# Optimization experiments

Hardware: AMD Instinct MI355X
Metric: run time of the kernel (lower is better)

## Reference

```python
import jax, jax.numpy as jnp
import numpy as np

B, T, M, E = 2, 2048, 1024, 8
CAP = (2 * B * T) // E  # GShard top-2 capacity = 2*S/E = 1024


def setup_inputs() -> dict:
    key = jax.random.key(0)
    k1, k2, k3 = jax.random.split(key, 3)
    x = jax.random.normal(k1, (B, T, M), jnp.float32)
    wg = jax.random.normal(k2, (M, E), jnp.float32) * 0.02
    expert_w = jax.random.normal(k3, (E, M, M), jnp.float32) * 0.02
    expert_b = jnp.zeros((E, M), jnp.float32)
    return {"x": x, "wg": wg, "expert_w": expert_w, "expert_b": expert_b}


def _top2_gate(x2, wg, capacity):
    """fairseq/GShard Top2Gate (deterministic second-expert, no jitter).
    Returns (l_aux, combine_weights[S,E,C], dispatch_mask[S,E,C] bool)."""
    S = x2.shape[0]
    num_experts = wg.shape[1]
    logits = x2 @ wg                                  # [S, E]
    gates = jax.nn.softmax(logits, axis=-1)           # [S, E]
    # top-1 expert
    idx1 = jnp.argmax(gates, axis=1)
    mask1 = jax.nn.one_hot(idx1, num_experts, dtype=jnp.int32)
    # top-2 expert: argmax over logits with top-1 masked out
    neg_inf = jnp.finfo(logits.dtype).min
    logits_wo1 = jnp.where(mask1.astype(bool), neg_inf, logits)
    idx2 = jnp.argmax(logits_wo1, axis=1)
    mask2 = jax.nn.one_hot(idx2, num_experts, dtype=jnp.int32)
    # positions within each expert's buffer
    loc1 = jnp.cumsum(mask1, axis=0) - 1              # [S, E]
    loc2 = jnp.cumsum(mask2, axis=0) - 1 + jnp.sum(mask1, axis=0, keepdims=True)
    # load-balancing auxiliary loss
    me = jnp.mean(gates, axis=0)
    ce = jnp.mean(mask1.astype(gates.dtype), axis=0)
    l_aux = jnp.mean(me * ce) * (num_experts * num_experts)
    # drop tokens over capacity
    mask1 = mask1 * (loc1 < capacity).astype(jnp.int32)
    mask2 = mask2 * (loc2 < capacity).astype(jnp.int32)
    loc1_s = jnp.sum(loc1 * mask1, axis=1)            # [S]
    loc2_s = jnp.sum(loc2 * mask2, axis=1)
    m1f = mask1.astype(gates.dtype)
    m2f = mask2.astype(gates.dtype)
    gates1_s = jnp.sum(gates * m1f, axis=1)
    gates2_s = jnp.sum(gates * m2f, axis=1)
    denom = gates1_s + gates2_s
    denom = jnp.clip(denom, jnp.finfo(gates.dtype).eps, None)
    gates1 = gates1_s / denom
    gates2 = gates2_s / denom
    loc1_oh = jax.nn.one_hot(loc1_s, capacity, dtype=gates.dtype)  # [S, C]
    loc2_oh = jax.nn.one_hot(loc2_s, capacity, dtype=gates.dtype)
    combine1 = gates1[:, None, None] * m1f[:, :, None] * loc1_oh[:, None, :]
    combine2 = gates2[:, None, None] * m2f[:, :, None] * loc2_oh[:, None, :]
    combine_weights = combine1 + combine2             # [S, E, C]
    dispatch_mask = combine_weights > 0               # bool [S, E, C]
    return l_aux, combine_weights, dispatch_mask


def reference(x, wg, expert_w, expert_b):
    b, t, d = x.shape
    x2 = x.reshape(-1, d)                             # [S, M]
    l_aux, cw, dm = _top2_gate(x2, wg, CAP)
    dmf = dm.astype(x.dtype)                          # [S, E, C]
    # dispatch: (E*C, S) @ (S, M) -> per-expert token buffers [E, C, M]
    dispatched = jnp.einsum('sec,sm->ecm', dmf, x2)
    # per-expert Linear (single device: all experts local, all-to-all = identity)
    expert_out = jnp.einsum('ecm,emn->ecn', dispatched, expert_w) + expert_b[:, None, :]
    # combine: (S, E*C) @ (E*C, M) -> [S, M]
    combined = jnp.einsum('sec,ecm->sm', cw, expert_out)
    return combined.reshape(b, t, d), l_aux
```

## Files before the change

### kernel.cpp

```cpp
#include <hip/hip_runtime.h>

typedef unsigned short u16;
typedef short v8s __attribute__((ext_vector_type(8)));
typedef float v4f __attribute__((ext_vector_type(4)));

#define S_TOK 4096
#define MDIM  1024
#define NEXP  8
#define CAPN  1024

__device__ __forceinline__ u16 f2bf(float f) {
  unsigned int u = __float_as_uint(f);
  u += 0x7FFFu + ((u >> 16) & 1u);
  return (u16)(u >> 16);
}

__device__ __forceinline__ void gll16(const void* g, void* l) {
  __builtin_amdgcn_global_load_lds(
      (const __attribute__((address_space(1))) void*)g,
      (__attribute__((address_space(3))) void*)l, 16, 0, 0);
}

__global__ __launch_bounds__(256) void init_kernel(int* slot_token, u16* zrow, float* gsum) {
  int gid = blockIdx.x * 256 + threadIdx.x;
  if (gid < NEXP * CAPN) slot_token[gid] = -1;
  if (gid < MDIM) zrow[gid] = 0;
  if (gid < NEXP) gsum[gid] = 0.f;
}

__global__ __launch_bounds__(256) void transw_kernel(const float* __restrict__ w,
                                                     u16* __restrict__ wT) {
  int b  = blockIdx.x;
  int e  = b >> 8;
  int mt = (b >> 4) & 15;
  int nt = b & 15;
  __shared__ float tile[64][65];
  const float* src = w + (size_t)e * MDIM * MDIM;
  u16* dst = wT + (size_t)e * MDIM * MDIM;
  int tid = threadIdx.x;
#pragma unroll
  for (int i = 0; i < 16; i++) {
    int idx = tid + i * 256;
    int r = idx >> 6, c = idx & 63;
    tile[r][c] = src[(size_t)(mt * 64 + r) * MDIM + nt * 64 + c];
  }
  __syncthreads();
#pragma unroll
  for (int i = 0; i < 16; i++) {
    int idx = tid + i * 256;
    int r = idx >> 6, c = idx & 63;
    dst[(size_t)(nt * 64 + r) * MDIM + mt * 64 + c] = f2bf(tile[c][r]);
  }
}

__global__ __launch_bounds__(256) void gate_kernel(const float* __restrict__ x,
                                                   const float* __restrict__ wg,
                                                   u16* __restrict__ xbf,
                                                   int4* __restrict__ grec,
                                                   float* __restrict__ gsum) {
  __shared__ float wls[NEXP * MDIM];
  __shared__ float gsh[4][NEXP];
  int tid = threadIdx.x;
  for (int i = tid; i < NEXP * MDIM; i += 256) {
    int m = i >> 3, e = i & 7;
    wls[e * MDIM + m] = wg[i];
  }
  __syncthreads();
  int wave = tid >> 6, lane = tid & 63;
  int s = blockIdx.x * 4 + wave;
  const float* xr = x + (size_t)s * MDIM;
  u16* xw = xbf + (size_t)s * MDIM;
  float acc[NEXP];
#pragma unroll
  for (int e = 0; e < NEXP; e++) acc[e] = 0.f;
#pragma unroll
  for (int j = 0; j < 16; j++) {
    int m = j * 64 + lane;
    float xv = xr[m];
    xw[m] = f2bf(xv);
#pragma unroll
    for (int e = 0; e < NEXP; e++) acc[e] = fmaf(xv, wls[e * MDIM + m], acc[e]);
  }
#pragma unroll
  for (int off = 32; off > 0; off >>= 1)
#pragma unroll
    for (int e = 0; e < NEXP; e++) acc[e] += __shfl_xor(acc[e], off, 64);

  if (lane == 0) {
    float mx = acc[0];
#pragma unroll
    for (int e = 1; e < NEXP; e++) mx = fmaxf(mx, acc[e]);
    float ex[NEXP], sum = 0.f;
#pragma unroll
    for (int e = 0; e < NEXP; e++) { ex[e] = expf(acc[e] - mx); sum += ex[e]; }
    float inv = 1.f / sum;
    int e1 = 0; float b1 = acc[0];
#pragma unroll
    for (int e = 1; e < NEXP; e++) if (acc[e] > b1) { b1 = acc[e]; e1 = e; }
    int e2 = -1; float b2 = -3.4e38f;
#pragma unroll
    for (int e = 0; e < NEXP; e++) if (e != e1 && acc[e] > b2) { b2 = acc[e]; e2 = e; }
    grec[s] = make_int4(e1, e2, __float_as_int(ex[e1] * inv), __float_as_int(ex[e2] * inv));
#pragma unroll
    for (int e = 0; e < NEXP; e++) gsh[wave][e] = ex[e] * inv;
  }
  __syncthreads();
  if (tid < NEXP)
    atomicAdd(&gsum[tid], gsh[0][tid] + gsh[1][tid] + gsh[2][tid] + gsh[3][tid]);
}

__global__ __launch_bounds__(1024) void scan_kernel(const int4* __restrict__ grec,
                                                    int4* __restrict__ trec,
                                                    int* __restrict__ slot_token,
                                                    const float* __restrict__ gsum,
                                                    float* __restrict__ out) {
  __shared__ unsigned long long scanA[1024], scanB[1024];
  int t = threadIdx.x;
  int e1[4], e2[4];
  float g1[4], g2[4];
#pragma unroll
  for (int i = 0; i < 4; i++) {
    int4 r = grec[t * 4 + i];
    e1[i] = r.x; e2[i] = r.y;
    g1[i] = __int_as_float(r.z); g2[i] = __int_as_float(r.w);
  }
  unsigned long long a0 = 0, b0 = 0;
#pragma unroll
  for (int i = 0; i < 4; i++) {
    if (e1[i] < 4) a0 += 1ULL << (e1[i] * 16); else b0 += 1ULL << ((e1[i] - 4) * 16);
  }
  scanA[t] = a0; scanB[t] = b0;
  __syncthreads();
  for (int off = 1; off < 1024; off <<= 1) {
    unsigned long long pa = 0, pb = 0;
    if (t >= off) { pa = scanA[t - off]; pb = scanB[t - off]; }
    __syncthreads();
    if (t >= off) { scanA[t] += pa; scanB[t] += pb; }
    __syncthreads();
  }
  unsigned long long ea = scanA[t] - a0, eb2 = scanB[t] - b0;
  unsigned long long ta = scanA[1023], tb = scanB[1023];
  int base[NEXP], cnt1[NEXP];
#pragma unroll
  for (int e = 0; e < 4; e++) {
    base[e]     = (int)((ea  >> (e * 16)) & 0xFFFF);
    base[4 + e] = (int)((eb2 >> (e * 16)) & 0xFFFF);
    cnt1[e]     = (int)((ta  >> (e * 16)) & 0xFFFF);
    cnt1[4 + e] = (int)((tb  >> (e * 16)) & 0xFFFF);
  }
  int loc1[4];
#pragma unroll
  for (int i = 0; i < 4; i++) {
    int l = 0;
#pragma unroll
    for (int q = 0; q < NEXP; q++) if (q == e1[i]) { l = base[q]; base[q] = l + 1; }
    loc1[i] = l;
  }
  __syncthreads();
  a0 = 0; b0 = 0;
#pragma unroll
  for (int i = 0; i < 4; i++) {
    if (e2[i] < 4) a0 += 1ULL << (e2[i] * 16); else b0 += 1ULL << ((e2[i] - 4) * 16);
  }
  scanA[t] = a0; scanB[t] = b0;
  __syncthreads();
  for (int off = 1; off < 1024; off <<= 1) {
    unsigned long long pa = 0, pb = 0;
    if (t >= off) { pa = scanA[t - off]; pb = scanB[t - off]; }
    __syncthreads();
    if (t >= off) { scanA[t] += pa; scanB[t] += pb; }
    __syncthreads();
  }
  ea = scanA[t] - a0; eb2 = scanB[t] - b0;
#pragma unroll
  for (int e = 0; e < 4; e++) {
    base[e]     = (int)((ea  >> (e * 16)) & 0xFFFF);
    base[4 + e] = (int)((eb2 >> (e * 16)) & 0xFFFF);
  }
#pragma unroll
  for (int i = 0; i < 4; i++) {
    int s = t * 4 + i;
    int l2 = 0;
#pragma unroll
    for (int q = 0; q < NEXP; q++) if (q == e2[i]) { l2 = base[q]; base[q] = l2 + 1; }
    int loc2 = l2 + cnt1[e2[i]];
    bool k1 = loc1[i] < CAPN;
    bool k2 = loc2 < CAPN;
    float g1s = k1 ? g1[i] : 0.f;
    float g2s = k2 ? g2[i] : 0.f;
    float denom = fmaxf(g1s + g2s, 1.1920929e-7f);
    float gn1 = g1s / denom, gn2 = g2s / denom;
    int slot1 = k1 ? e1[i] * CAPN + loc1[i] : -1;
    int slot2 = k2 ? e2[i] * CAPN + loc2 : -1;
    trec[s] = make_int4(slot1, slot2, __float_as_int(gn1), __float_as_int(gn2));
    if (k1) slot_token[slot1] = s;
    if (k2) slot_token[slot2] = s;
  }
  if (t == 0) {
    float acc = 0.f;
#pragma unroll
    for (int e = 0; e < NEXP; e++) acc += gsum[e] * (float)cnt1[e];
    out[(size_t)S_TOK * MDIM] = 8.f * acc / (4096.f * 4096.f);
  }
}

__global__ __launch_bounds__(256, 2) void expert_gemm(const u16* __restrict__ xbf,
                                                      const u16* __restrict__ wT,
                                                      const int* __restrict__ slot_token,
                                                      const u16* __restrict__ zrow,
                                                      float* __restrict__ eout) {
  __shared__ __align__(16) u16 As[128 * 64];
  __shared__ __align__(16) u16 Bs[128 * 64];
  const int tid  = threadIdx.x;
  const int e    = blockIdx.x >> 6;
  const int tile = blockIdx.x & 63;
  const int tm   = (tile >> 3) << 7;
  const int tn   = (tile & 7) << 7;
  const int lane = tid & 63;
  const int wave = tid >> 6;
  const int wr = wave >> 1, wc = wave & 1;

  const u16* srcA[4];
  const u16* srcB[4];
#pragma unroll
  for (int it = 0; it < 4; ++it) {
    int off = tid * 16 + it * 4096;
    int row = off >> 7;
    int kb  = off & 127;
    int st  = slot_token[e * CAPN + tm + row];
    srcA[it] = (st >= 0 ? xbf + (size_t)st * MDIM : zrow) + (kb >> 1);
    srcB[it] = wT + (size_t)e * MDIM * MDIM + (size_t)(tn + row) * MDIM + (kb >> 1);
  }
  char* ldsA = (char*)As;
  char* ldsB = (char*)Bs;

  v4f acc[4][4];
#pragma unroll
  for (int i = 0; i < 4; i++)
#pragma unroll
    for (int j = 0; j < 4; j++) acc[i][j] = (v4f){0.f, 0.f, 0.f, 0.f};

  for (int k0 = 0; k0 < MDIM; k0 += 64) {
    __syncthreads();
#pragma unroll
    for (int it = 0; it < 4; ++it)
      gll16(srcA[it] + k0, ldsA + tid * 16 + it * 4096);
#pragma unroll
    for (int it = 0; it < 4; ++it)
      gll16(srcB[it] + k0, ldsB + tid * 16 + it * 4096);
    __syncthreads();

    const v8s* Ap = (const v8s*)As;
    const v8s* Bp = (const v8s*)Bs;
#pragma unroll
    for (int ks = 0; ks < 2; ++ks) {
      v8s af[4], bf[4];
#pragma unroll
      for (int i = 0; i < 4; i++)
        af[i] = Ap[(wr * 64 + i * 16 + (lane & 15)) * 8 + ks * 4 + (lane >> 4)];
#pragma unroll
      for (int j = 0; j < 4; j++)
        bf[j] = Bp[(wc * 64 + j * 16 + (lane & 15)) * 8 + ks * 4 + (lane >> 4)];
#pragma unroll
      for (int i = 0; i < 4; i++)
#pragma unroll
        for (int j = 0; j < 4; j++)
          acc[i][j] = __builtin_amdgcn_mfma_f32_16x16x32_bf16(af[i], bf[j], acc[i][j], 0, 0, 0);
    }
  }

  float* outp = eout + (size_t)e * CAPN * MDIM;
#pragma unroll
  for (int i = 0; i < 4; i++) {
#pragma unroll
    for (int r = 0; r < 4; r++) {
      int row = tm + wr * 64 + i * 16 + (lane >> 4) * 4 + r;
#pragma unroll
      for (int j = 0; j < 4; j++) {
        int col = tn + wc * 64 + j * 16 + (lane & 15);
        outp[(size_t)row * MDIM + col] = acc[i][j][r];
      }
    }
  }
}

__global__ __launch_bounds__(256) void combine_kernel(const float* __restrict__ eout,
                                                      const int4* __restrict__ trec,
                                                      const float* __restrict__ bias,
                                                      float* __restrict__ out) {
  int s = blockIdx.x;
  int tid = threadIdx.x;
  int4 r = trec[s];
  float g1 = __int_as_float(r.z), g2 = __int_as_float(r.w);
  const float4* e4 = (const float4*)eout;
  const float4* b4 = (const float4*)bias;
  float yx = 0.f, yy = 0.f, yz = 0.f, yw = 0.f;
  if (r.x >= 0) {
    float4 o = e4[(size_t)r.x * 256 + tid];
    float4 b = b4[(size_t)(r.x >> 10) * 256 + tid];
    yx += g1 * (o.x + b.x); yy += g1 * (o.y + b.y);
    yz += g1 * (o.z + b.z); yw += g1 * (o.w + b.w);
  }
  if (r.y >= 0) {
    float4 o = e4[(size_t)r.y * 256 + tid];
    float4 b = b4[(size_t)(r.y >> 10) * 256 + tid];
    yx += g2 * (o.x + b.x); yy += g2 * (o.y + b.y);
    yz += g2 * (o.z + b.z); yw += g2 * (o.w + b.w);
  }
  float4 res; res.x = yx; res.y = yy; res.z = yz; res.w = yw;
  ((float4*)out)[(size_t)s * 256 + tid] = res;
}

extern "C" void kernel_launch(void* const* d_in, const int* in_sizes, int n_in,
                              void* d_out, int out_size, void* d_ws, size_t ws_size,
                              hipStream_t stream) {
  (void)in_sizes; (void)n_in; (void)out_size; (void)ws_size;
  const float* x  = (const float*)d_in[0];
  const float* wg = (const float*)d_in[1];
  const float* ew = (const float*)d_in[2];
  const float* eb = (const float*)d_in[3];
  float* out = (float*)d_out;

  char* ws = (char*)d_ws;
  u16*   xbf  = (u16*)(ws + 0);
  u16*   wT   = (u16*)(ws + 8388608);
  float* eout = (float*)(ws + 25165824);
  u16*   zrow = (u16*)(ws + 58720256);
  int4*  grec = (int4*)(ws + 58722304);
  int4*  trec = (int4*)(ws + 58787840);
  int*   slot = (int*)(ws + 58853376);
  float* gsum = (float*)(ws + 58886144);

  init_kernel<<<32, 256, 0, stream>>>(slot, zrow, gsum);
  transw_kernel<<<2048, 256, 0, stream>>>(ew, wT);
  gate_kernel<<<1024, 256, 0, stream>>>(x, wg, xbf, grec, gsum);
  scan_kernel<<<1, 1024, 0, stream>>>(grec, trec, slot, gsum, out);
  expert_gemm<<<512, 256, 0, stream>>>(xbf, wT, slot, zrow, eout);
  combine_kernel<<<4096, 256, 0, stream>>>(eout, trec, eb, out);
}
```

Measured before the change: 163.1 us.

## Drop init kernel, use wave-shuffle scan, and store expert outputs as bf16 with fused bias

Removes the init kernel by moving slot_token/zrow initialization into the scan kernel, and replaces gate atomics with per-block partial sums reduced in the scan. The scan kernel swaps two LDS Hillis-Steele scans with many barriers for a single combined wave-shuffle scan over both top-1 and top-2 counts. The expert GEMM now adds bias and writes bf16 outputs, halving intermediate store/load traffic for the combine kernel. The bf16 intermediate adds rounding error to the output.

```diff
diff --git a/kernel.cpp b/kernel.cpp
--- a/kernel.cpp
+++ b/kernel.cpp
@@ -1,6 +1,8 @@
 #include <hip/hip_runtime.h>
 
 typedef unsigned short u16;
+typedef unsigned int u32;
+typedef unsigned long long u64;
 typedef short v8s __attribute__((ext_vector_type(8)));
 typedef float v4f __attribute__((ext_vector_type(4)));
 
@@ -10,22 +12,17 @@
 #define CAPN  1024
 
 __device__ __forceinline__ u16 f2bf(float f) {
-  unsigned int u = __float_as_uint(f);
+  u32 u = __float_as_uint(f);
   u += 0x7FFFu + ((u >> 16) & 1u);
   return (u16)(u >> 16);
 }
-
+__device__ __forceinline__ float bf2f(u16 h) {
+  return __uint_as_float(((u32)h) << 16);
+}
 __device__ __forceinline__ void gll16(const void* g, void* l) {
   __builtin_amdgcn_global_load_lds(
       (const __attribute__((address_space(1))) void*)g,
       (__attribute__((address_space(3))) void*)l, 16, 0, 0);
-}
-
-__global__ __launch_bounds__(256) void init_kernel(int* slot_token, u16* zrow, float* gsum) {
-  int gid = blockIdx.x * 256 + threadIdx.x;
-  if (gid < NEXP * CAPN) slot_token[gid] = -1;
-  if (gid < MDIM) zrow[gid] = 0;
-  if (gid < NEXP) gsum[gid] = 0.f;
 }
 
 __global__ __launch_bounds__(256) void transw_kernel(const float* __restrict__ w,
@@ -57,7 +54,7 @@
                                                    const float* __restrict__ wg,
                                                    u16* __restrict__ xbf,
                                                    int4* __restrict__ grec,
-                                                   float* __restrict__ gsum) {
+                                                   float* __restrict__ gpart) {
   __shared__ float wls[NEXP * MDIM];
   __shared__ float gsh[4][NEXP];
   int tid = threadIdx.x;
@@ -106,92 +103,103 @@
   }
   __syncthreads();
   if (tid < NEXP)
-    atomicAdd(&gsum[tid], gsh[0][tid] + gsh[1][tid] + gsh[2][tid] + gsh[3][tid]);
+    gpart[blockIdx.x * NEXP + tid] = gsh[0][tid] + gsh[1][tid] + gsh[2][tid] + gsh[3][tid];
 }
 
 __global__ __launch_bounds__(1024) void scan_kernel(const int4* __restrict__ grec,
                                                     int4* __restrict__ trec,
                                                     int* __restrict__ slot_token,
-                                                    const float* __restrict__ gsum,
+                                                    const float* __restrict__ gpart,
+                                                    u16* __restrict__ zrow,
                                                     float* __restrict__ out) {
-  __shared__ unsigned long long scanA[1024], scanB[1024];
-  int t = threadIdx.x;
-  int e1[4], e2[4];
-  float g1[4], g2[4];
+  __shared__ u64 wtot[16][4];
+  __shared__ float gred[16][NEXP];
+  int t = threadIdx.x, lane = t & 63, wave = t >> 6;
+
+#pragma unroll
+  for (int i = 0; i < 8; i++) slot_token[t + i * 1024] = -1;
+  zrow[t] = 0;
+
+  float4 p0 = ((const float4*)gpart)[t * 2];
+  float4 p1 = ((const float4*)gpart)[t * 2 + 1];
+  float gs[NEXP] = {p0.x, p0.y, p0.z, p0.w, p1.x, p1.y, p1.z, p1.w};
+#pragma unroll
+  for (int off = 32; off > 0; off >>= 1)
+#pragma unroll
+    for (int e = 0; e < NEXP; e++) gs[e] += __shfl_xor(gs[e], off, 64);
+  if (lane == 0)
+#pragma unroll
+    for (int e = 0; e < NEXP; e++) gred[wave][e] = gs[e];
+
+  int4 r[4];
+#pragma unroll
+  for (int i = 0; i < 4; i++) r[i] = grec[t * 4 + i];
+
+  u64 a1 = 0, b1 = 0, a2 = 0, b2 = 0;
 #pragma unroll
   for (int i = 0; i < 4; i++) {
-    int4 r = grec[t * 4 + i];
-    e1[i] = r.x; e2[i] = r.y;
-    g1[i] = __int_as_float(r.z); g2[i] = __int_as_float(r.w);
-  }
-  unsigned long long a0 = 0, b0 = 0;
-#pragma unroll
-  for (int i = 0; i < 4; i++) {
-    if (e1[i] < 4) a0 += 1ULL << (e1[i] * 16); else b0 += 1ULL << ((e1[i] - 4) * 16);
-  }
-  scanA[t] = a0; scanB[t] = b0;
-  __syncthreads();
-  for (int off = 1; off < 1024; off <<= 1) {
-    unsigned long long pa = 0, pb = 0;
-    if (t >= off) { pa = scanA[t - off]; pb = scanB[t - off]; }
-    __syncthreads();
-    if (t >= off) { scanA[t] += pa; scanB[t] += pb; }
-    __syncthreads();
-  }
-  unsigned long long ea = scanA[t] - a0, eb2 = scanB[t] - b0;
-  unsigned long long ta = scanA[1023], tb = scanB[1023];
-  int base[NEXP], cnt1[NEXP];
+    int x1 = r[i].x, x2 = r[i].y;
+    if (x1 < 4) a1 += 1ULL << (x1 * 16); else b1 += 1ULL << ((x1 - 4) * 16);
+    if (x2 < 4) a2 += 1ULL << (x2 * 16); else b2 += 1ULL << ((x2 - 4) * 16);
+  }
+  u64 ia1 = a1, ib1 = b1, ia2 = a2, ib2 = b2;
+#pragma unroll
+  for (int off = 1; off < 64; off <<= 1) {
+    u64 s1 = __shfl_up(a1, off, 64), s2 = __shfl_up(b1, off, 64);
+    u64 s3 = __shfl_up(a2, off, 64), s4 = __shfl_up(b2, off, 64);
+    if (lane >= off) { a1 += s1; b1 += s2; a2 += s3; b2 += s4; }
+  }
+  if (lane == 63) { wtot[wave][0] = a1; wtot[wave][1] = b1; wtot[wave][2] = a2; wtot[wave][3] = b2; }
+  __syncthreads();
+  if (t < 16) {
+    u64 v0 = wtot[t][0], v1 = wtot[t][1], v2 = wtot[t][2], v3 = wtot[t][3];
+#pragma unroll
+    for (int off = 1; off < 16; off <<= 1) {
+      u64 s0 = __shfl_up(v0, off, 64), s1 = __shfl_up(v1, off, 64);
+      u64 s2 = __shfl_up(v2, off, 64), s3 = __shfl_up(v3, off, 64);
+      if (t >= off) { v0 += s0; v1 += s1; v2 += s2; v3 += s3; }
+    }
+    wtot[t][0] = v0; wtot[t][1] = v1; wtot[t][2] = v2; wtot[t][3] = v3;
+  }
+  __syncthreads();
+  u64 o1 = 0, o2 = 0, o3 = 0, o4 = 0;
+  if (wave > 0) { o1 = wtot[wave - 1][0]; o2 = wtot[wave - 1][1]; o3 = wtot[wave - 1][2]; o4 = wtot[wave - 1][3]; }
+  u64 ea  = a1 + o1 - ia1;
+  u64 eb  = b1 + o2 - ib1;
+  u64 ea2 = a2 + o3 - ia2;
+  u64 eb2 = b2 + o4 - ib2;
+  u64 ta = wtot[15][0], tb = wtot[15][1];
+
+  int base1[NEXP], base2[NEXP], cnt1[NEXP];
 #pragma unroll
   for (int e = 0; e < 4; e++) {
-    base[e]     = (int)((ea  >> (e * 16)) & 0xFFFF);
-    base[4 + e] = (int)((eb2 >> (e * 16)) & 0xFFFF);
-    cnt1[e]     = (int)((ta  >> (e * 16)) & 0xFFFF);
-    cnt1[4 + e] = (int)((tb  >> (e * 16)) & 0xFFFF);
-  }
-  int loc1[4];
-#pragma unroll
-  for (int i = 0; i < 4; i++) {
-    int l = 0;
-#pragma unroll
-    for (int q = 0; q < NEXP; q++) if (q == e1[i]) { l = base[q]; base[q] = l + 1; }
-    loc1[i] = l;
-  }
-  __syncthreads();
-  a0 = 0; b0 = 0;
-#pragma unroll
-  for (int i = 0; i < 4; i++) {
-    if (e2[i] < 4) a0 += 1ULL << (e2[i] * 16); else b0 += 1ULL << ((e2[i] - 4) * 16);
-  }
-  scanA[t] = a0; scanB[t] = b0;
-  __syncthreads();
-  for (int off = 1; off < 1024; off <<= 1) {
-    unsigned long long pa = 0, pb = 0;
-    if (t >= off) { pa = scanA[t - off]; pb = scanB[t - off]; }
-    __syncthreads();
-    if (t >= off) { scanA[t] += pa; scanB[t] += pb; }
-    __syncthreads();
-  }
-  ea = scanA[t] - a0; eb2 = scanB[t] - b0;
-#pragma unroll
-  for (int e = 0; e < 4; e++) {
-    base[e]     = (int)((ea  >> (e * 16)) & 0xFFFF);
-    base[4 + e] = (int)((eb2 >> (e * 16)) & 0xFFFF);
+    base1[e]     = (int)((ea  >> (e * 16)) & 0xFFFF);
+    base1[4 + e] = (int)((eb  >> (e * 16)) & 0xFFFF);
+    base2[e]     = (int)((ea2 >> (e * 16)) & 0xFFFF);
+    base2[4 + e] = (int)((eb2 >> (e * 16)) & 0xFFFF);
+    cnt1[e]      = (int)((ta  >> (e * 16)) & 0xFFFF);
+    cnt1[4 + e]  = (int)((tb  >> (e * 16)) & 0xFFFF);
   }
 #pragma unroll
   for (int i = 0; i < 4; i++) {
     int s = t * 4 + i;
-    int l2 = 0;
-#pragma unroll
-    for (int q = 0; q < NEXP; q++) if (q == e2[i]) { l2 = base[q]; base[q] = l2 + 1; }
-    int loc2 = l2 + cnt1[e2[i]];
-    bool k1 = loc1[i] < CAPN;
+    int e1 = r[i].x, e2 = r[i].y;
+    float g1 = __int_as_float(r[i].z), g2 = __int_as_float(r[i].w);
+    int l1 = 0, l2 = 0;
+#pragma unroll
+    for (int q = 0; q < NEXP; q++) {
+      if (q == e1) { l1 = base1[q]; base1[q] = l1 + 1; }
+      if (q == e2) { l2 = base2[q]; base2[q] = l2 + 1; }
+    }
+    int loc2 = l2 + cnt1[e2];
+    bool k1 = l1 < CAPN;
     bool k2 = loc2 < CAPN;
-    float g1s = k1 ? g1[i] : 0.f;
-    float g2s = k2 ? g2[i] : 0.f;
+    float g1s = k1 ? g1 : 0.f;
+    float g2s = k2 ? g2 : 0.f;
     float denom = fmaxf(g1s + g2s, 1.1920929e-7f);
     float gn1 = g1s / denom, gn2 = g2s / denom;
-    int slot1 = k1 ? e1[i] * CAPN + loc1[i] : -1;
-    int slot2 = k2 ? e2[i] * CAPN + loc2 : -1;
+    int slot1 = k1 ? e1 * CAPN + l1 : -1;
+    int slot2 = k2 ? e2 * CAPN + loc2 : -1;
     trec[s] = make_int4(slot1, slot2, __float_as_int(gn1), __float_as_int(gn2));
     if (k1) slot_token[slot1] = s;
     if (k2) slot_token[slot2] = s;
@@ -199,7 +207,11 @@
   if (t == 0) {
     float acc = 0.f;
 #pragma unroll
-    for (int e = 0; e < NEXP; e++) acc += gsum[e] * (float)cnt1[e];
+    for (int e = 0; e < NEXP; e++) {
+      float g = 0.f;
+      for (int w = 0; w < 16; w++) g += gred[w][e];
+      acc += g * (float)cnt1[e];
+    }
     out[(size_t)S_TOK * MDIM] = 8.f * acc / (4096.f * 4096.f);
   }
 }
@@ -208,7 +220,8 @@
                                                       const u16* __restrict__ wT,
                                                       const int* __restrict__ slot_token,
                                                       const u16* __restrict__ zrow,
-                                                      float* __restrict__ eout) {
+                                                      const float* __restrict__ bias,
+                                                      u16* __restrict__ eoutb) {
   __shared__ __align__(16) u16 As[128 * 64];
   __shared__ __align__(16) u16 Bs[128 * 64];
   const int tid  = threadIdx.x;
@@ -254,60 +267,58 @@
     const v8s* Bp = (const v8s*)Bs;
 #pragma unroll
     for (int ks = 0; ks < 2; ++ks) {
-      v8s af[4], bf[4];
+      v8s af[4], bfr[4];
 #pragma unroll
       for (int i = 0; i < 4; i++)
         af[i] = Ap[(wr * 64 + i * 16 + (lane & 15)) * 8 + ks * 4 + (lane >> 4)];
 #pragma unroll
       for (int j = 0; j < 4; j++)
-        bf[j] = Bp[(wc * 64 + j * 16 + (lane & 15)) * 8 + ks * 4 + (lane >> 4)];
+        bfr[j] = Bp[(wc * 64 + j * 16 + (lane & 15)) * 8 + ks * 4 + (lane >> 4)];
 #pragma unroll
       for (int i = 0; i < 4; i++)
 #pragma unroll
         for (int j = 0; j < 4; j++)
-          acc[i][j] = __builtin_amdgcn_mfma_f32_16x16x32_bf16(af[i], bf[j], acc[i][j], 0, 0, 0);
-    }
-  }
-
-  float* outp = eout + (size_t)e * CAPN * MDIM;
+          acc[i][j] = __builtin_amdgcn_mfma_f32_16x16x32_bf16(af[i], bfr[j], acc[i][j], 0, 0, 0);
+    }
+  }
+
+  const float* bp = bias + (size_t)e * MDIM;
+  float bv[4];
+#pragma unroll
+  for (int j = 0; j < 4; j++) bv[j] = bp[tn + wc * 64 + j * 16 + (lane & 15)];
+  u16* outp = eoutb + (size_t)e * CAPN * MDIM;
 #pragma unroll
   for (int i = 0; i < 4; i++) {
 #pragma unroll
-    for (int r = 0; r < 4; r++) {
-      int row = tm + wr * 64 + i * 16 + (lane >> 4) * 4 + r;
+    for (int rr = 0; rr < 4; rr++) {
+      int row = tm + wr * 64 + i * 16 + (lane >> 4) * 4 + rr;
 #pragma unroll
       for (int j = 0; j < 4; j++) {
         int col = tn + wc * 64 + j * 16 + (lane & 15);
-        outp[(size_t)row * MDIM + col] = acc[i][j][r];
+        outp[(size_t)row * MDIM + col] = f2bf(acc[i][j][rr] + bv[j]);
       }
     }
   }
 }
 
-__global__ __launch_bounds__(256) void combine_kernel(const float* __restrict__ eout,
+__global__ __launch_bounds__(256) void combine_kernel(const u16* __restrict__ eoutb,
                                                       const int4* __restrict__ trec,
-                                                      const float* __restrict__ bias,
                                                       float* __restrict__ out) {
   int s = blockIdx.x;
   int tid = threadIdx.x;
   int4 r = trec[s];
   float g1 = __int_as_float(r.z), g2 = __int_as_float(r.w);
-  const float4* e4 = (const float4*)eout;
-  const float4* b4 = (const float4*)bias;
-  float yx = 0.f, yy = 0.f, yz = 0.f, yw = 0.f;
+  float4 res = make_float4(0.f, 0.f, 0.f, 0.f);
   if (r.x >= 0) {
-    float4 o = e4[(size_t)r.x * 256 + tid];
-    float4 b = b4[(size_t)(r.x >> 10) * 256 + tid];
-    yx += g1 * (o.x + b.x); yy += g1 * (o.y + b.y);
-    yz += g1 * (o.z + b.z); yw += g1 * (o.w + b.w);
+    ushort4 o = ((const ushort4*)(eoutb + (size_t)r.x * MDIM))[tid];
+    res.x += g1 * bf2f(o.x); res.y += g1 * bf2f(o.y);
+    res.z += g1 * bf2f(o.z); res.w += g1 * bf2f(o.w);
   }
   if (r.y >= 0) {
-    float4 o = e4[(size_t)r.y * 256 + tid];
-    float4 b = b4[(size_t)(r.y >> 10) * 256 + tid];
-    yx += g2 * (o.x + b.x); yy += g2 * (o.y + b.y);
-    yz += g2 * (o.z + b.z); yw += g2 * (o.w + b.w);
-  }
-  float4 res; res.x = yx; res.y = yy; res.z = yz; res.w = yw;
+    ushort4 o = ((const ushort4*)(eoutb + (size_t)r.y * MDIM))[tid];
+    res.x += g2 * bf2f(o.x); res.y += g2 * bf2f(o.y);
+    res.z += g2 * bf2f(o.z); res.w += g2 * bf2f(o.w);
+  }
   ((float4*)out)[(size_t)s * 256 + tid] = res;
 }
 
@@ -322,19 +333,18 @@
   float* out = (float*)d_out;
 
   char* ws = (char*)d_ws;
-  u16*   xbf  = (u16*)(ws + 0);
-  u16*   wT   = (u16*)(ws + 8388608);
-  float* eout = (float*)(ws + 25165824);
-  u16*   zrow = (u16*)(ws + 58720256);
-  int4*  grec = (int4*)(ws + 58722304);
-  int4*  trec = (int4*)(ws + 58787840);
-  int*   slot = (int*)(ws + 58853376);
-  float* gsum = (float*)(ws + 58886144);
-
-  init_kernel<<<32, 256, 0, stream>>>(slot, zrow, gsum);
+  u16*   xbf   = (u16*)(ws + 0);
+  u16*   wT    = (u16*)(ws + 8388608);
+  u16*   eoutb = (u16*)(ws + 25165824);
+  u16*   zrow  = (u16*)(ws + 41943040);
+  int4*  grec  = (int4*)(ws + 41945088);
+  int4*  trec  = (int4*)(ws + 42010624);
+  int*   slot  = (int*)(ws + 42076160);
+  float* gpart = (float*)(ws + 42108928);
+
   transw_kernel<<<2048, 256, 0, stream>>>(ew, wT);
-  gate_kernel<<<1024, 256, 0, stream>>>(x, wg, xbf, grec, gsum);
-  scan_kernel<<<1, 1024, 0, stream>>>(grec, trec, slot, gsum, out);
-  expert_gemm<<<512, 256, 0, stream>>>(xbf, wT, slot, zrow, eout);
-  combine_kernel<<<4096, 256, 0, stream>>>(eout, trec, eb, out);
-}
+  gate_kernel<<<1024, 256, 0, stream>>>(x, wg, xbf, grec, gpart);
+  scan_kernel<<<1, 1024, 0, stream>>>(grec, trec, slot, gpart, zrow, out);
+  expert_gemm<<<512, 256, 0, stream>>>(xbf, wT, slot, zrow, eb, eoutb);
+  combine_kernel<<<4096, 256, 0, stream>>>(eoutb, trec, out);
+}
```

Result: faster. 147.8 us (-9.4%).
